# Optimization experiments

Hardware: AMD Instinct MI355X
Metric: run time of the kernel (lower is better)

The kernel has to match this reference:

```python
import math
import jax, jax.numpy as jnp
import numpy as np

ANCHORS_SETTINGS = (
    dict(layer='p3', stride=32, size=48, scale=[2 ** (1.0 / 3.0), 2 ** (2.0 / 3.0)], aspect_ratio=[0.667, 1, 1.5]),
    dict(layer='p4', stride=64, size=96, scale=[2 ** (1.0 / 3.0), 2 ** (2.0 / 3.0)], aspect_ratio=[0.667, 1, 1.5]),
    dict(layer='p5', stride=128, size=192, scale=[1, 2 ** (1.0 / 3.0), 2 ** (2.0 / 3.0)], aspect_ratio=[0.667, 1, 1.5]),
)


def anchor_configs():
    # 21 static (kernel, stride, padding) configs, in the exact counter order of
    # weighted_anchor_aggregator (p3 x6, p4 x6, p5 x9).
    cfgs = []
    for info in ANCHORS_SETTINGS:
        stride, size = info['stride'], info['size']
        for scale in info['scale']:
            for ar in info['aspect_ratio']:
                kernel = (int(size * scale / float(ar) ** 0.5), int(size * scale * float(ar) ** 0.5))
                padding = (math.ceil((kernel[0] - stride) / 2.0), math.ceil((kernel[1] - stride) / 2.0))
                cfgs.append((kernel, (stride, stride), padding))
    return cfgs


def extract_weighted_patches(x, weights, kernel, stride, padding):
    # x: (B,H,W,C); weights: (B,k,gh,gw). Vectorized equivalent of the original
    # lax.scan over per-position dynamic_slice gathers:
    #   acc = sum_{i,j} weights[:,:,i,j] (x) x_pad[:, i*s : i*s+kh, j*s : j*s+kw, :]
    b = x.shape[0]
    _, k, gh, gw = weights.shape
    xp = jnp.pad(x, ((0, 0),
                     (padding[0], padding[0] + kernel[0]),
                     (padding[1], padding[1] + kernel[1]),
                     (0, 0)))
    rows = jnp.arange(gh)[:, None] * stride[0] + jnp.arange(kernel[0])[None, :]  # (gh, kh)
    cols = jnp.arange(gw)[:, None] * stride[1] + jnp.arange(kernel[1])[None, :]  # (gw, kw)
    # gather all strided patches: (B, gh, kh, gw, kw, C)
    patches = xp[:, rows][:, :, :, cols]
    # weighted sum over grid positions -> (B, k, kh, kw, C)
    return jnp.einsum('bkij,bihjwc->bkhwc', weights, patches)


def _aggregate(x, weights_p3, weights_p4, weights_p5):
    weights = ([weights_p3[:, a] for a in range(weights_p3.shape[1])]
               + [weights_p4[:, a] for a in range(weights_p4.shape[1])]
               + [weights_p5[:, a] for a in range(weights_p5.shape[1])])
    b, k = weights[0].shape[0], weights[0].shape[1]
    acc = jnp.zeros((b * k, 224, 224, 3), x.dtype)
    for w, (kernel, stride, padding) in zip(weights, anchor_configs()):
        agg = extract_weighted_patches(x, w, kernel, stride, padding)
        agg = agg.reshape(b * k, kernel[0], kernel[1], 3)
        acc = acc + jax.image.resize(agg, (b * k, 224, 224, 3), 'bilinear')
    return acc


def setup_inputs() -> dict:
    key = jax.random.key(0)
    k0, k1, k2, k3 = jax.random.split(key, 4)
    B, K = 8, 4
    return {
        'x': jax.random.normal(k0, (B, 448, 448, 3), jnp.float32),
        'weights_p3': jax.random.uniform(k1, (B, 6, K, 14, 14), jnp.float32),
        'weights_p4': jax.random.uniform(k2, (B, 6, K, 7, 7), jnp.float32),
        'weights_p5': jax.random.uniform(k3, (B, 9, K, 4, 4), jnp.float32),
    }


def reference(x, weights_p3, weights_p4, weights_p5):
    return _aggregate(x, weights_p3, weights_p4, weights_p5)
```

## Files before the change

kernel.cpp:

```cpp
#include <hip/hip_runtime.h>
#include <math.h>


#define BATCH 8
#define KK 4
#define OUT_HW 224
#define IMG_HW 448
#define NCFG 21

#define WTBL_BYTES (NCFG * 2 * OUT_HW * 16)
#define ITBL_BYTES (NCFG * 2 * OUT_HW * 4)
#define WT_OFF_BYTES (WTBL_BYTES + ITBL_BYTES)
#define WT_F4 12912
#define AGG_OFF_BYTES (WT_OFF_BYTES + WT_F4 * 16)

#define RZ_GRID (14 * 14 * 16)

typedef float v2f __attribute__((ext_vector_type(2)));

static constexpr int cKH[NCFG]  = {74,60,49,93,76,62, 148,120,98,186,152,124,
                                   235,192,156,296,241,197,373,304,248};
static constexpr int cKW[NCFG]  = {49,60,74,62,76,93, 98,120,148,124,152,186,
                                   156,192,235,197,241,296,248,304,373};
static constexpr int cMTH[NCFG] = {2,2,2,2,2,2, 2,2,2,2,2,2, 3,2,2,3,3,2,4,3,3};
static constexpr int cMTW[NCFG] = {2,2,2,2,2,2, 2,2,2,2,2,2, 2,2,3,2,3,3,3,3,4};

__host__ __device__ constexpr int ckwp(int c) { return cKW[c] + (cKW[c] & 1); }
__host__ __device__ constexpr long cwsoff(int c, int g) {
    long o = 0;
    for (int k = g; k < c; ++k) o += (long)cKH[k] * ckwp(k) * (BATCH * KK);
    return o;
}

struct ACfg {
    int kh, kw, kwp, p0, p1;
    int layer;
    int ns;
    int wt_off;
    int ws_off;
    int block_start;
    int blocks_per_img;
};

struct AggArgs {
    ACfg e[NCFG];
    int n;
};

struct TablesArgs { int kh[NCFG]; int kw[NCFG]; };

struct TrArgs {
    int layer[NCFG];
    int anchor[NCFG];
    int gsz[NCFG];
    int wt_off[NCFG];
};

struct F3 { float a, b, c; };

__device__ inline unsigned int bf16_rne(float f) {
    unsigned int u = __float_as_uint(f);
    return (u + 0x7fffu + ((u >> 16) & 1u)) >> 16;
}

__global__ __launch_bounds__(256) void init_tables(float4* __restrict__ wtbl,
                                                   int* __restrict__ itbl,
                                                   TablesArgs t) {
    int cfg = blockIdx.x >> 1;
    int dim = blockIdx.x & 1;
    int o = threadIdx.x;
    if (o >= OUT_HW) return;
    int n = dim ? t.kw[cfg] : t.kh[cfg];

    float inv = (float)(1.0 / ((double)OUT_HW / (double)n));
    float ks  = inv > 1.f ? inv : 1.f;
    float rks = 1.f / ks;
    float sf  = ((float)o + 0.5f) * inv - 0.5f;
    int i0 = (int)ceilf(sf - ks);  if (i0 < 0) i0 = 0;
    int i1 = (int)floorf(sf + ks); if (i1 > n - 1) i1 = n - 1;
    float sum = 0.f;
    for (int i = i0; i <= i1; ++i) {
        float v = 1.f - fabsf((float)i - sf) * rks;
        sum += (v > 0.f ? v : 0.f);
    }
    float rsum = 1.f / sum;
    float w[4];
#pragma unroll
    for (int d = 0; d < 4; ++d) {
        int i = i0 + d;
        float v = 0.f;
        if (i <= i1) {
            v = 1.f - fabsf((float)i - sf) * rks;
            v = (v > 0.f ? v : 0.f) * rsum;
        }
        w[d] = v;
    }
    int idx = cfg * (2 * OUT_HW) + dim * OUT_HW + o;
    wtbl[idx] = make_float4(w[0], w[1], w[2], w[3]);
    itbl[idx] = i0;
}

__global__ __launch_bounds__(256) void transpose_w(
        const float* __restrict__ wp3, const float* __restrict__ wp4,
        const float* __restrict__ wp5, float4* __restrict__ wT, TrArgs t) {
    int cfg = blockIdx.x;
    int b = blockIdx.y;
    int gsz = t.gsz[cfg];
    const float* base;
    int A;
    if (t.layer[cfg] == 0)      { base = wp3; A = 6; }
    else if (t.layer[cfg] == 1) { base = wp4; A = 6; }
    else                        { base = wp5; A = 9; }
    const float* src = base + (size_t)(b * A + t.anchor[cfg]) * (KK * gsz);
    for (int g = threadIdx.x; g < gsz; g += 256) {
        wT[t.wt_off[cfg] + b * gsz + g] =
            make_float4(src[0 * gsz + g], src[1 * gsz + g],
                        src[2 * gsz + g], src[3 * gsz + g]);
    }
}

template <int GH, int GW, int STRIDE, int L2S>
__device__ inline void agg_body(const ACfg& c, int b, int h, int slot,
                                const float* __restrict__ xb,
                                const float4* __restrict__ wlds,
                                uint2* __restrict__ agg) {
    const int w0 = (((slot >> L2S) << (L2S + 1)) | (slot & (STRIDE - 1)));
    const int w1 = w0 + STRIDE;
    const bool two = w1 < c.kw;

    v2f acc2[4][3];
#pragma unroll
    for (int k = 0; k < 4; ++k)
#pragma unroll
        for (int ch = 0; ch < 3; ++ch) { acc2[k][ch].x = 0.f; acc2[k][ch].y = 0.f; }

    const int rb = h - c.p0;
    int ilo = rb >= 0 ? 0 : (-rb + STRIDE - 1) / STRIDE;
    int ihi = (IMG_HW - 1 - rb) / STRIDE;
    if (ihi > GH - 1) ihi = GH - 1;

    const int cb = w0 - c.p1;

    int  cof[GW + 1];
    bool ok [GW + 1];
#pragma unroll
    for (int jj = 0; jj <= GW; ++jj) {
        int col = cb + jj * STRIDE;
        ok[jj] = (unsigned)col < (unsigned)IMG_HW;
        unsigned cc = (unsigned)col;
        if (cc > (unsigned)(IMG_HW - 1)) cc = (unsigned)(IMG_HW - 1);
        cof[jj] = (int)cc * 3;
    }

#pragma unroll 1
    for (int i = ilo; i <= ihi; ++i) {
        const float* xr = xb + (size_t)(rb + i * STRIDE) * (IMG_HW * 3);
        const float4* wrow = wlds + i * GW;

        float px[GW + 1][3];
#pragma unroll
        for (int jj = 0; jj <= GW; ++jj) {
            F3 v = *(const F3*)(xr + cof[jj]);
            px[jj][0] = ok[jj] ? v.a : 0.f;
            px[jj][1] = ok[jj] ? v.b : 0.f;
            px[jj][2] = ok[jj] ? v.c : 0.f;
        }

#pragma unroll
        for (int j = 0; j < GW; ++j) {
            float4 wk = wrow[j];
            v2f d0 = {px[j][0], px[j + 1][0]};
            v2f d1 = {px[j][1], px[j + 1][1]};
            v2f d2 = {px[j][2], px[j + 1][2]};
            v2f wv0 = {wk.x, wk.x};
            v2f wv1 = {wk.y, wk.y};
            v2f wv2 = {wk.z, wk.z};
            v2f wv3 = {wk.w, wk.w};
            acc2[0][0] = __builtin_elementwise_fma(wv0, d0, acc2[0][0]);
            acc2[0][1] = __builtin_elementwise_fma(wv0, d1, acc2[0][1]);
            acc2[0][2] = __builtin_elementwise_fma(wv0, d2, acc2[0][2]);
            acc2[1][0] = __builtin_elementwise_fma(wv1, d0, acc2[1][0]);
            acc2[1][1] = __builtin_elementwise_fma(wv1, d1, acc2[1][1]);
            acc2[1][2] = __builtin_elementwise_fma(wv1, d2, acc2[1][2]);
            acc2[2][0] = __builtin_elementwise_fma(wv2, d0, acc2[2][0]);
            acc2[2][1] = __builtin_elementwise_fma(wv2, d1, acc2[2][1]);
            acc2[2][2] = __builtin_elementwise_fma(wv2, d2, acc2[2][2]);
            acc2[3][0] = __builtin_elementwise_fma(wv3, d0, acc2[3][0]);
            acc2[3][1] = __builtin_elementwise_fma(wv3, d1, acc2[3][1]);
            acc2[3][2] = __builtin_elementwise_fma(wv3, d2, acc2[3][2]);
        }
    }

    const int npix = c.kh * c.kwp;
    size_t pb0 = (size_t)c.ws_off
               + ((size_t)b * npix + (size_t)h * c.kwp + w0) * KK;
    {
        uint4 s0, s1;
        s0.x = bf16_rne(acc2[0][0].x) | (bf16_rne(acc2[0][1].x) << 16);
        s0.y = bf16_rne(acc2[0][2].x);
        s0.z = bf16_rne(acc2[1][0].x) | (bf16_rne(acc2[1][1].x) << 16);
        s0.w = bf16_rne(acc2[1][2].x);
        s1.x = bf16_rne(acc2[2][0].x) | (bf16_rne(acc2[2][1].x) << 16);
        s1.y = bf16_rne(acc2[2][2].x);
        s1.z = bf16_rne(acc2[3][0].x) | (bf16_rne(acc2[3][1].x) << 16);
        s1.w = bf16_rne(acc2[3][2].x);
        *(uint4*)(agg + pb0)     = s0;
        *(uint4*)(agg + pb0 + 2) = s1;
    }
    if (two) {
        size_t pb1 = pb0 + (size_t)STRIDE * KK;
        uint4 s0, s1;
        s0.x = bf16_rne(acc2[0][0].y) | (bf16_rne(acc2[0][1].y) << 16);
        s0.y = bf16_rne(acc2[0][2].y);
        s0.z = bf16_rne(acc2[1][0].y) | (bf16_rne(acc2[1][1].y) << 16);
        s0.w = bf16_rne(acc2[1][2].y);
        s1.x = bf16_rne(acc2[2][0].y) | (bf16_rne(acc2[2][1].y) << 16);
        s1.y = bf16_rne(acc2[2][2].y);
        s1.z = bf16_rne(acc2[3][0].y) | (bf16_rne(acc2[3][1].y) << 16);
        s1.w = bf16_rne(acc2[3][2].y);
        *(uint4*)(agg + pb1)     = s0;
        *(uint4*)(agg + pb1 + 2) = s1;
    }
}

__device__ inline void agg_top(int bid, const float* __restrict__ x,
                               const float4* __restrict__ wT,
                               uint2* __restrict__ agg, const AggArgs& a,
                               float4* wlds, int tid) {
    int ci = 0;
    while (ci + 1 < a.n && bid >= a.e[ci + 1].block_start) ci++;
    const ACfg c = a.e[ci];
    int local = bid - c.block_start;
    int b     = local & 7;
    int sblk  = local >> 3;

    const int gsz = (c.layer == 0) ? 196 : (c.layer == 1) ? 49 : 16;
    for (int t = tid; t < gsz; t += 256)
        wlds[t] = wT[c.wt_off + b * gsz + t];
    __syncthreads();

    int pidx = sblk * 256 + tid;
    if (pidx >= c.kh * c.ns) return;
    int h    = pidx / c.ns;
    int slot = pidx - h * c.ns;

    const float* __restrict__ xb = x + (size_t)b * (IMG_HW * IMG_HW * 3);
    if (c.layer == 0)      agg_body<14, 14, 32, 5>(c, b, h, slot, xb, wlds, agg);
    else if (c.layer == 1) agg_body<7, 7, 64, 6>(c, b, h, slot, xb, wlds, agg);
    else                   agg_body<4, 4, 128, 7>(c, b, h, slot, xb, wlds, agg);
}

__global__ __launch_bounds__(256, 3) void agg_all(
        const float* __restrict__ x,
        const float4* __restrict__ wT,
        uint2* __restrict__ agg,
        AggArgs a) {
    __shared__ float4 wlds[196];
    agg_top(blockIdx.x, x, wT, agg, a, wlds, (int)threadIdx.x);
}

template <int TH, int TW, int KH_, int KW_, int KWP_>
__device__ inline void taps_ct2(const uint2* __restrict__ pb,
                                int i0, int j0,
                                float4 wh4, float4 ww4,
                                v2f (&a)[3]) {
    const float* wh = (const float*)&wh4;
    const float* ww = (const float*)&ww4;
    uint4 v[TH][TW];
#pragma unroll
    for (int d = 0; d < TH; ++d) {
        int gi = i0 + d;
        if (gi > KH_ - 1) gi = KH_ - 1;
        const uint2* rp = pb + (size_t)gi * (KWP_ * KK);
#pragma unroll
        for (int e = 0; e < TW; ++e) {
            int gj = j0 + e;
            if (gj > KW_ - 1) gj = KW_ - 1;
            v[d][e] = *(const uint4*)(rp + gj * KK);
        }
    }
#pragma unroll
    for (int d = 0; d < TH; ++d) {
        v2f r0 = {0.f, 0.f}, r1 = {0.f, 0.f}, r2 = {0.f, 0.f};
#pragma unroll
        for (int e = 0; e < TW; ++e) {
            uint4 q = v[d][e];
            v2f c0, c1, c2;
            c0.x = __uint_as_float(q.x << 16);
            c0.y = __uint_as_float(q.z << 16);
            c1.x = __uint_as_float(q.x & 0xffff0000u);
            c1.y = __uint_as_float(q.z & 0xffff0000u);
            c2.x = __uint_as_float(q.y << 16);
            c2.y = __uint_as_float(q.w << 16);
            v2f w2 = {ww[e], ww[e]};
            r0 = __builtin_elementwise_fma(w2, c0, r0);
            r1 = __builtin_elementwise_fma(w2, c1, r1);
            r2 = __builtin_elementwise_fma(w2, c2, r2);
        }
        v2f h2 = {wh[d], wh[d]};
        a[0] = __builtin_elementwise_fma(h2, r0, a[0]);
        a[1] = __builtin_elementwise_fma(h2, r1, a[1]);
        a[2] = __builtin_elementwise_fma(h2, r2, a[2]);
    }
}

template <int C, int CEND, int CSTART>
__device__ inline void do_rounds(const uint2* __restrict__ agg,
                                 const float4* __restrict__ wlds,
                                 const int* __restrict__ ilds,
                                 int b, int kp, int tx, int ty,
                                 v2f (&a)[3]) {
    if constexpr (C < CEND) {
        constexpr int li  = C - CSTART;
        constexpr int kh  = cKH[C];
        constexpr int kw  = cKW[C];
        constexpr int kwp = ckwp(C);
        constexpr long wso = cwsoff(C, CSTART);
        float4 wh4 = wlds[li * 32 + ty];
        float4 ww4 = wlds[li * 32 + 16 + tx];
        int i0 = ilds[li * 32 + ty];
        int j0 = ilds[li * 32 + 16 + tx];
        const uint2* pb = agg + wso
                        + (size_t)b * ((size_t)kh * kwp * KK) + kp * 2;
        taps_ct2<cMTH[C], cMTW[C], kh, kw, kwp>(pb, i0, j0, wh4, ww4, a);
        do_rounds<C + 1, CEND, CSTART>(agg, wlds, ilds, b, kp, tx, ty, a);
    }
}

template <int CSTART, int CEND>
__device__ inline void rz_top(const uint2* __restrict__ agg,
                              const float4* __restrict__ wtbl,
                              const int* __restrict__ itbl,
                              float* __restrict__ out, int accumulate,
                              int bx, int by, int zz, int tid,
                              float4* wlds, int* ilds) {
    constexpr int NC = CEND - CSTART;
    const int tx = tid & 15;
    const int ty = tid >> 4;
    const int xo = bx * 16 + tx;
    const int yo = by * 16 + ty;
    const int b  = zz >> 1;
    const int kp = zz & 1;

    for (int e = tid; e < NC * 32; e += 256) {
        int ci  = e >> 5;
        int r   = e & 31;
        int isW = r >> 4;
        int idx = r & 15;
        int base_o = isW ? (bx * 16) : (by * 16);
        int src = (CSTART + ci) * (2 * OUT_HW) + isW * OUT_HW + base_o + idx;
        wlds[ci * 32 + r] = wtbl[src];
        ilds[ci * 32 + r] = itbl[src];
    }
    __syncthreads();

    size_t obA = ((((size_t)(b * KK + kp * 2)) * OUT_HW + yo) * OUT_HW + xo) * 3;
    size_t obB = obA + (size_t)OUT_HW * OUT_HW * 3;

    v2f a[3];
    if (accumulate) {
        a[0].x = out[obA + 0]; a[0].y = out[obB + 0];
        a[1].x = out[obA + 1]; a[1].y = out[obB + 1];
        a[2].x = out[obA + 2]; a[2].y = out[obB + 2];
    } else {
        a[0] = v2f{0.f, 0.f}; a[1] = v2f{0.f, 0.f}; a[2] = v2f{0.f, 0.f};
    }

    do_rounds<CSTART, CEND, CSTART>(agg, wlds, ilds, b, kp, tx, ty, a);

    out[obA + 0] = a[0].x; out[obA + 1] = a[1].x; out[obA + 2] = a[2].x;
    out[obB + 0] = a[0].y; out[obB + 1] = a[1].y; out[obB + 2] = a[2].y;
}

template <int CSTART, int CEND>
__global__ __launch_bounds__(256, 4) void resize_static(
        const uint2* __restrict__ agg,
        const float4* __restrict__ wtbl,
        const int* __restrict__ itbl,
        float* __restrict__ out,
        int accumulate) {
    constexpr int NC = CEND - CSTART;
    __shared__ float4 wlds[NC * 32];
    __shared__ int    ilds[NC * 32];
    rz_top<CSTART, CEND>(agg, wtbl, itbl, out, accumulate,
                         (int)blockIdx.x, (int)blockIdx.y, (int)blockIdx.z,
                         (int)threadIdx.x, wlds, ilds);
}

template <int CSTART, int CEND>
__global__ __launch_bounds__(256, 3) void fused_k(
        const float* __restrict__ x,
        const float4* __restrict__ wT,
        uint2* __restrict__ aggW,
        AggArgs a, int naggBlocks,
        const uint2* __restrict__ aggR,
        const float4* __restrict__ wtbl,
        const int* __restrict__ itbl,
        float* __restrict__ out,
        int accumulate) {
    constexpr int NC = CEND - CSTART;
    __shared__ float4 wldsA[196];
    __shared__ float4 wldsR[NC * 32];
    __shared__ int    ildsR[NC * 32];
    const int tid = (int)threadIdx.x;
    if ((int)blockIdx.x < naggBlocks) {
        agg_top((int)blockIdx.x, x, wT, aggW, a, wldsA, tid);
    } else {
        int rid = (int)blockIdx.x - naggBlocks;
        int bx = rid % 14;
        int t2 = rid / 14;
        int by = t2 % 14;
        int zz = t2 / 14;
        rz_top<CSTART, CEND>(aggR, wtbl, itbl, out, accumulate,
                             bx, by, zz, tid, wldsR, ildsR);
    }
}

extern "C" void kernel_launch(void* const* d_in, const int* in_sizes, int n_in,
                              void* d_out, int out_size, void* d_ws, size_t ws_size,
                              hipStream_t stream) {
    const float* x   = (const float*)d_in[0];
    const float* wp3 = (const float*)d_in[1];
    const float* wp4 = (const float*)d_in[2];
    const float* wp5 = (const float*)d_in[3];
    float* out = (float*)d_out;
    float4* wtbl = (float4*)d_ws;
    int*    itbl = (int*)((char*)d_ws + WTBL_BYTES);
    float4* wT   = (float4*)((char*)d_ws + WT_OFF_BYTES);
    uint2*  agg  = (uint2*)((char*)d_ws + AGG_OFF_BYTES);

    struct { int stride, size, nscale; double scales[3]; int gh; } layers[3] = {
        {32, 48, 2, {pow(2.0, 1.0 / 3.0), pow(2.0, 2.0 / 3.0), 0.0}, 14},
        {64, 96, 2, {pow(2.0, 1.0 / 3.0), pow(2.0, 2.0 / 3.0), 0.0}, 7},
        {128, 192, 3, {1.0, pow(2.0, 1.0 / 3.0), pow(2.0, 2.0 / 3.0)}, 4},
    };
    const double ars[3] = {0.667, 1.0, 1.5};

    struct HostCfg {
        int kh, kw, kwp, stride, p0, p1, gh, gw, layer, anchor, wt_off;
        int ns, blocks_per_img;
    } cfg[NCFG];
    TablesArgs ta;
    TrArgs tr;
    int nc = 0, wt_run = 0;
    for (int L = 0; L < 3; ++L) {
        int anchor = 0;
        for (int si = 0; si < layers[L].nscale; ++si) {
            for (int ai = 0; ai < 3; ++ai) {
                double ss = (double)layers[L].size * layers[L].scales[si];
                double sq = pow(ars[ai], 0.5);
                int kh = (int)(ss / sq);
                int kw = (int)(ss * sq);
                HostCfg& e = cfg[nc];
                e.kh = kh; e.kw = kw;
                e.kwp = kw + (kw & 1);
                e.stride = layers[L].stride;
                e.p0 = (int)ceil((double)(kh - layers[L].stride) / 2.0);
                e.p1 = (int)ceil((double)(kw - layers[L].stride) / 2.0);
                e.gh = layers[L].gh; e.gw = layers[L].gh;
                e.layer = L; e.anchor = anchor++;
                int s = e.stride;
                int q = kw / s, r = kw % s;
                e.ns = ((q + 1) / 2) * s + ((q % 2 == 0) ? r : 0);
                e.blocks_per_img = (kh * e.ns + 255) / 256;
                e.wt_off = wt_run;
                int gsz = e.gh * e.gw;
                wt_run += BATCH * gsz;
                ta.kh[nc] = kh; ta.kw[nc] = kw;
                tr.layer[nc] = L; tr.anchor[nc] = e.anchor;
                tr.gsz[nc] = gsz; tr.wt_off[nc] = e.wt_off;
                ++nc;
            }
        }
    }

    init_tables<<<NCFG * 2, 256, 0, stream>>>(wtbl, itbl, ta);
    transpose_w<<<dim3(NCFG, BATCH), 256, 0, stream>>>(wp3, wp4, wp5, wT, tr);

    auto build = [&](int gstart, int gend, AggArgs& aa) -> int {
        aa.n = 0;
        int ablocks = 0;
        size_t off = 0;
        for (int c = gstart; c < gend; ++c) {
            ACfg& lc = aa.e[aa.n++];
            lc.kh = cfg[c].kh; lc.kw = cfg[c].kw; lc.kwp = cfg[c].kwp;
            lc.p0 = cfg[c].p0; lc.p1 = cfg[c].p1;
            lc.layer = cfg[c].layer;
            lc.ns = cfg[c].ns;
            lc.wt_off = cfg[c].wt_off;
            lc.ws_off = (int)off;
            lc.block_start = ablocks;
            lc.blocks_per_img = cfg[c].blocks_per_img;
            ablocks += cfg[c].blocks_per_img * BATCH;
            off += (size_t)cfg[c].kh * cfg[c].kwp * (BATCH * KK);
        }
        return ablocks;
    };
    auto gpx = [&](int gstart, int gend) -> size_t {
        size_t p = 0;
        for (int c = gstart; c < gend; ++c)
            p += (size_t)cfg[c].kh * cfg[c].kwp;
        return p * (BATCH * KK);
    };

    size_t pxG0 = gpx(0, 15), pxG1 = gpx(15, 19), pxG2 = gpx(19, 21);
    size_t pxA = pxG0 > pxG2 ? pxG0 : pxG2;
    size_t pxB = pxG1;
    bool can_overlap =
        (size_t)AGG_OFF_BYTES + (pxA + pxB) * sizeof(uint2) <= ws_size;

    if (can_overlap) {
        uint2* bufA = agg;
        uint2* bufB = agg + pxA;
        AggArgs a0, a1, a2;
        int n0 = build(0, 15, a0);
        int n1 = build(15, 19, a1);
        int n2 = build(19, 21, a2);

        agg_all<<<n0, 256, 0, stream>>>(x, wT, bufA, a0);
        fused_k<0, 15><<<n1 + RZ_GRID, 256, 0, stream>>>(
            x, wT, bufB, a1, n1, bufA, wtbl, itbl, out, 0);
        fused_k<15, 19><<<n2 + RZ_GRID, 256, 0, stream>>>(
            x, wT, bufA, a2, n2, bufB, wtbl, itbl, out, 1);
        resize_static<19, 21><<<dim3(14, 14, 16), 256, 0, stream>>>(
            bufA, wtbl, itbl, out, 1);
    } else {
        dim3 rgrid(14, 14, 16);
        AggArgs aa;
        int nb;
        nb = build(0, 15, aa);
        agg_all<<<nb, 256, 0, stream>>>(x, wT, agg, aa);
        resize_static<0, 15><<<rgrid, 256, 0, stream>>>(agg, wtbl, itbl, out, 0);
        nb = build(15, 19, aa);
        agg_all<<<nb, 256, 0, stream>>>(x, wT, agg, aa);
        resize_static<15, 19><<<rgrid, 256, 0, stream>>>(agg, wtbl, itbl, out, 1);
        nb = build(19, 21, aa);
        agg_all<<<nb, 256, 0, stream>>>(x, wT, agg, aa);
        resize_static<19, 21><<<rgrid, 256, 0, stream>>>(agg, wtbl, itbl, out, 1);
    }
    (void)in_sizes; (void)n_in; (void)out_size;
}
```

Before: 267.7 us.

## Pre-pad input columns into workspace buffer and remap resize block ordering

Adds a kernel that copies the input into a column-padded buffer (128 zero columns on the left, width 768), so the aggregation inner loop drops its per-pixel bounds checks and selects. Resize blocks switch to a 1D grid with a decomposition that interleaves the batch/anchor pairs across consecutive block ids, which changes the order in which tiles are scheduled. The cost is an extra kernel launch, about 44 MB of workspace traffic for the padded copy, and a larger workspace requirement. That larger requirement can make the overlapped path fall back to the serial one if the workspace is too small.

Result: slower. 278.5 us (+4.0%).

```diff
diff --git a/kernel.cpp b/kernel.cpp
--- a/kernel.cpp
+++ b/kernel.cpp
@@ -8,11 +8,17 @@
 #define IMG_HW 448
 #define NCFG 21
 
+#define XP_W 768
+#define XP_ROWF (XP_W * 3)
+
 #define WTBL_BYTES (NCFG * 2 * OUT_HW * 16)
 #define ITBL_BYTES (NCFG * 2 * OUT_HW * 4)
 #define WT_OFF_BYTES (WTBL_BYTES + ITBL_BYTES)
 #define WT_F4 12912
-#define AGG_OFF_BYTES (WT_OFF_BYTES + WT_F4 * 16)
+#define XPAD_OFF_BYTES (WT_OFF_BYTES + WT_F4 * 16)
+#define XPAD_FLOATS_IMG (IMG_HW * XP_ROWF)
+#define XPAD_BYTES (BATCH * XPAD_FLOATS_IMG * 4)
+#define AGG_OFF_BYTES (XPAD_OFF_BYTES + XPAD_BYTES)
 
 #define RZ_GRID (14 * 14 * 16)
 
@@ -119,9 +125,33 @@
     }
 }
 
+__global__ __launch_bounds__(256) void build_xpad(
+        const float* __restrict__ x, float* __restrict__ xpad) {
+    int f4 = (int)blockIdx.x * 256 + (int)threadIdx.x;
+    int f0 = f4 * 4;
+    int b   = f0 / XPAD_FLOATS_IMG;
+    int rem = f0 - b * XPAD_FLOATS_IMG;
+    int row = rem / XP_ROWF;
+    int cf  = rem - row * XP_ROWF;
+    float4 v;
+    float* vv = (float*)&v;
+#pragma unroll
+    for (int q = 0; q < 4; ++q) {
+        int cfq = cf + q;
+        int px = cfq / 3;
+        int ch = cfq - px * 3;
+        float val = 0.f;
+        int xc = px - 128;
+        if ((unsigned)xc < (unsigned)IMG_HW)
+            val = x[((size_t)b * IMG_HW + row) * (IMG_HW * 3) + xc * 3 + ch];
+        vv[q] = val;
+    }
+    *(float4*)(xpad + ((size_t)b * IMG_HW + row) * XP_ROWF + cf) = v;
+}
+
 template <int GH, int GW, int STRIDE, int L2S>
 __device__ inline void agg_body(const ACfg& c, int b, int h, int slot,
-                                const float* __restrict__ xb,
+                                const float* __restrict__ xpb,
                                 const float4* __restrict__ wlds,
                                 uint2* __restrict__ agg) {
     const int w0 = (((slot >> L2S) << (L2S + 1)) | (slot & (STRIDE - 1)));
@@ -139,31 +169,28 @@
     int ihi = (IMG_HW - 1 - rb) / STRIDE;
     if (ihi > GH - 1) ihi = GH - 1;
 
-    const int cb = w0 - c.p1;
-
-    int  cof[GW + 1];
-    bool ok [GW + 1];
+    const int cb = w0 - c.p1 + 128;
+
+    int cof[GW + 1];
 #pragma unroll
     for (int jj = 0; jj <= GW; ++jj) {
         int col = cb + jj * STRIDE;
-        ok[jj] = (unsigned)col < (unsigned)IMG_HW;
-        unsigned cc = (unsigned)col;
-        if (cc > (unsigned)(IMG_HW - 1)) cc = (unsigned)(IMG_HW - 1);
-        cof[jj] = (int)cc * 3;
+        if (col > XP_W - 1) col = XP_W - 1;
+        cof[jj] = col * 3;
     }
 
 #pragma unroll 1
     for (int i = ilo; i <= ihi; ++i) {
-        const float* xr = xb + (size_t)(rb + i * STRIDE) * (IMG_HW * 3);
+        const float* xr = xpb + (size_t)(rb + i * STRIDE) * XP_ROWF;
         const float4* wrow = wlds + i * GW;
 
         float px[GW + 1][3];
 #pragma unroll
         for (int jj = 0; jj <= GW; ++jj) {
             F3 v = *(const F3*)(xr + cof[jj]);
-            px[jj][0] = ok[jj] ? v.a : 0.f;
-            px[jj][1] = ok[jj] ? v.b : 0.f;
-            px[jj][2] = ok[jj] ? v.c : 0.f;
+            px[jj][0] = v.a;
+            px[jj][1] = v.b;
+            px[jj][2] = v.c;
         }
 
 #pragma unroll
@@ -223,7 +250,7 @@
     }
 }
 
-__device__ inline void agg_top(int bid, const float* __restrict__ x,
+__device__ inline void agg_top(int bid, const float* __restrict__ xpad,
                                const float4* __restrict__ wT,
                                uint2* __restrict__ agg, const AggArgs& a,
                                float4* wlds, int tid) {
@@ -244,19 +271,19 @@
     int h    = pidx / c.ns;
     int slot = pidx - h * c.ns;
 
-    const float* __restrict__ xb = x + (size_t)b * (IMG_HW * IMG_HW * 3);
-    if (c.layer == 0)      agg_body<14, 14, 32, 5>(c, b, h, slot, xb, wlds, agg);
-    else if (c.layer == 1) agg_body<7, 7, 64, 6>(c, b, h, slot, xb, wlds, agg);
-    else                   agg_body<4, 4, 128, 7>(c, b, h, slot, xb, wlds, agg);
+    const float* __restrict__ xpb = xpad + (size_t)b * XPAD_FLOATS_IMG;
+    if (c.layer == 0)      agg_body<14, 14, 32, 5>(c, b, h, slot, xpb, wlds, agg);
+    else if (c.layer == 1) agg_body<7, 7, 64, 6>(c, b, h, slot, xpb, wlds, agg);
+    else                   agg_body<4, 4, 128, 7>(c, b, h, slot, xpb, wlds, agg);
 }
 
 __global__ __launch_bounds__(256, 3) void agg_all(
-        const float* __restrict__ x,
+        const float* __restrict__ xpad,
         const float4* __restrict__ wT,
         uint2* __restrict__ agg,
         AggArgs a) {
     __shared__ float4 wlds[196];
-    agg_top(blockIdx.x, x, wT, agg, a, wlds, (int)threadIdx.x);
+    agg_top(blockIdx.x, xpad, wT, agg, a, wlds, (int)threadIdx.x);
 }
 
 template <int TH, int TW, int KH_, int KW_, int KWP_>
@@ -327,6 +354,17 @@
     }
 }
 
+__device__ inline void rz_decomp(int abs_bid, int n0,
+                                 int& bx, int& by, int& zz) {
+    int pair = abs_bid & 7;
+    int tile = (abs_bid - n0) >> 3;
+    int q    = tile / 196;
+    int t    = tile - q * 196;
+    zz = pair * 2 + q;
+    by = t / 14;
+    bx = t - by * 14;
+}
+
 template <int CSTART, int CEND>
 __device__ inline void rz_top(const uint2* __restrict__ agg,
                               const float4* __restrict__ wtbl,
@@ -382,14 +420,15 @@
     constexpr int NC = CEND - CSTART;
     __shared__ float4 wlds[NC * 32];
     __shared__ int    ilds[NC * 32];
+    int bx, by, zz;
+    rz_decomp((int)blockIdx.x, 0, bx, by, zz);
     rz_top<CSTART, CEND>(agg, wtbl, itbl, out, accumulate,
-                         (int)blockIdx.x, (int)blockIdx.y, (int)blockIdx.z,
-                         (int)threadIdx.x, wlds, ilds);
+                         bx, by, zz, (int)threadIdx.x, wlds, ilds);
 }
 
 template <int CSTART, int CEND>
 __global__ __launch_bounds__(256, 3) void fused_k(
-        const float* __restrict__ x,
+        const float* __restrict__ xpad,
         const float4* __restrict__ wT,
         uint2* __restrict__ aggW,
         AggArgs a, int naggBlocks,
@@ -404,13 +443,10 @@
     __shared__ int    ildsR[NC * 32];
     const int tid = (int)threadIdx.x;
     if ((int)blockIdx.x < naggBlocks) {
-        agg_top((int)blockIdx.x, x, wT, aggW, a, wldsA, tid);
+        agg_top((int)blockIdx.x, xpad, wT, aggW, a, wldsA, tid);
     } else {
-        int rid = (int)blockIdx.x - naggBlocks;
-        int bx = rid % 14;
-        int t2 = rid / 14;
-        int by = t2 % 14;
-        int zz = t2 / 14;
+        int bx, by, zz;
+        rz_decomp((int)blockIdx.x, naggBlocks, bx, by, zz);
         rz_top<CSTART, CEND>(aggR, wtbl, itbl, out, accumulate,
                              bx, by, zz, tid, wldsR, ildsR);
     }
@@ -427,6 +463,7 @@
     float4* wtbl = (float4*)d_ws;
     int*    itbl = (int*)((char*)d_ws + WTBL_BYTES);
     float4* wT   = (float4*)((char*)d_ws + WT_OFF_BYTES);
+    float*  xpad = (float*)((char*)d_ws + XPAD_OFF_BYTES);
     uint2*  agg  = (uint2*)((char*)d_ws + AGG_OFF_BYTES);
 
     struct { int stride, size, nscale; double scales[3]; int gh; } layers[3] = {
@@ -476,6 +513,7 @@
 
     init_tables<<<NCFG * 2, 256, 0, stream>>>(wtbl, itbl, ta);
     transpose_w<<<dim3(NCFG, BATCH), 256, 0, stream>>>(wp3, wp4, wp5, wT, tr);
+    build_xpad<<<(BATCH * XPAD_FLOATS_IMG / 4) / 256, 256, 0, stream>>>(x, xpad);
 
     auto build = [&](int gstart, int gend, AggArgs& aa) -> int {
         aa.n = 0;
@@ -517,26 +555,25 @@
         int n1 = build(15, 19, a1);
         int n2 = build(19, 21, a2);
 
-        agg_all<<<n0, 256, 0, stream>>>(x, wT, bufA, a0);
+        agg_all<<<n0, 256, 0, stream>>>(xpad, wT, bufA, a0);
         fused_k<0, 15><<<n1 + RZ_GRID, 256, 0, stream>>>(
-            x, wT, bufB, a1, n1, bufA, wtbl, itbl, out, 0);
+            xpad, wT, bufB, a1, n1, bufA, wtbl, itbl, out, 0);
         fused_k<15, 19><<<n2 + RZ_GRID, 256, 0, stream>>>(
-            x, wT, bufA, a2, n2, bufB, wtbl, itbl, out, 1);
-        resize_static<19, 21><<<dim3(14, 14, 16), 256, 0, stream>>>(
+            xpad, wT, bufA, a2, n2, bufB, wtbl, itbl, out, 1);
+        resize_static<19, 21><<<RZ_GRID, 256, 0, stream>>>(
             bufA, wtbl, itbl, out, 1);
     } else {
-        dim3 rgrid(14, 14, 16);
         AggArgs aa;
         int nb;
         nb = build(0, 15, aa);
-        agg_all<<<nb, 256, 0, stream>>>(x, wT, agg, aa);
-        resize_static<0, 15><<<rgrid, 256, 0, stream>>>(agg, wtbl, itbl, out, 0);
+        agg_all<<<nb, 256, 0, stream>>>(xpad, wT, agg, aa);
+        resize_static<0, 15><<<RZ_GRID, 256, 0, stream>>>(agg, wtbl, itbl, out, 0);
         nb = build(15, 19, aa);
-        agg_all<<<nb, 256, 0, stream>>>(x, wT, agg, aa);
-        resize_static<15, 19><<<rgrid, 256, 0, stream>>>(agg, wtbl, itbl, out, 1);
+        agg_all<<<nb, 256, 0, stream>>>(xpad, wT, agg, aa);
+        resize_static<15, 19><<<RZ_GRID, 256, 0, stream>>>(agg, wtbl, itbl, out, 1);
         nb = build(19, 21, aa);
-        agg_all<<<nb, 256, 0, stream>>>(x, wT, agg, aa);
-        resize_static<19, 21><<<rgrid, 256, 0, stream>>>(agg, wtbl, itbl, out, 1);
+        agg_all<<<nb, 256, 0, stream>>>(xpad, wT, agg, aa);
+        resize_static<19, 21><<<RZ_GRID, 256, 0, stream>>>(agg, wtbl, itbl, out, 1);
     }
     (void)in_sizes; (void)n_in; (void)out_size;
 }
```
